# Kernel tuning notes

Measured on AMD Instinct MI355X. Metric: run time of the kernel, lower is better.

## Reference

```python
import jax, jax.numpy as jnp
import numpy as np
from jax import lax

EPS = 1e-5
K = 80000 // 16  # sample_pixels // 16 selected regions per image


def _conv(x, w):
    return lax.conv_general_dilated(x, w, (1, 1), 'VALID',
                                    dimension_numbers=('NHWC', 'HWIO', 'NHWC'))


def _bn(x, g, b, m, v):
    # Keras BatchNormalization in inference mode
    return (x - m) * (g * lax.rsqrt(v + EPS)) + b


def _crop(x, bi, iy, ix, size, pad):
    # tf.image.crop_and_resize with 'nearest' and integer-aligned boxes of span
    # (size+2*pad) reduces to a zero-padded window gather (out-of-bounds -> 0).
    S = size + 2 * pad
    xp = jnp.pad(x, ((0, 0), (pad, pad), (pad, pad), (0, 0)))
    rows = iy[:, None] * size + jnp.arange(S)[None, :]  # padded coords (offset -pad+pad)
    cols = ix[:, None] * size + jnp.arange(S)[None, :]
    return xp[bi[:, None, None], rows[:, :, None], cols[:, None, :], :]  # [N,S,S,C]


def _replace(x, y, bi, iy, ix):
    # scatter 4x4 patches y [N,4,4,C] back into x [B,H,W,C] at block (iy,ix)
    B, H, W, C = x.shape
    x6 = x.reshape(B, H // 4, 4, W // 4, 4, C).transpose(0, 1, 3, 2, 4, 5)
    x6 = x6.at[bi, iy, ix].set(y)
    return x6.transpose(0, 1, 3, 2, 4, 5).reshape(B, H, W, C)


def _forward(src, bgr, pha, fgr, err, hid,
             w1, g1, b1, m1, v1, w2, g2, b2, m2, v2,
             w3, g3, b3, m3, v3, w4, b4):
    B, Hf, Wf = src.shape[:3]
    Hh, Wh, Hq, Wq = Hf // 2, Wf // 2, Hf // 4, Wf // 4
    src_bgr = jnp.concatenate([src, bgr], axis=-1)

    # err already at quarter resolution -> tf bilinear resize is identity
    top_idx = lax.top_k(err[..., 0].reshape(B, -1), K)[1]  # [B,K]
    ref = jnp.zeros((B, Hq * Wq), err.dtype).at[jnp.arange(B)[:, None], top_idx].set(1.0)
    ref = ref.reshape(B, Hq, Wq, 1) * (err > 0).astype(err.dtype)

    bi = jnp.repeat(jnp.arange(B), K)          # [N] patch batch index, N = B*K
    iy = (top_idx // Wq).reshape(-1)
    ix = (top_idx % Wq).reshape(-1)

    x = jnp.concatenate([hid, pha, fgr], axis=-1)  # [B,Hq,Wq,36]
    x = jax.image.resize(x, (B, Hh, Wh, x.shape[-1]), 'bilinear')
    xp = _crop(x, bi, iy, ix, 2, 3)                # [N,8,8,36]
    yh = jax.image.resize(src_bgr, (B, Hh, Wh, 6), 'bilinear')
    yp = _crop(yh, bi, iy, ix, 2, 3)               # [N,8,8,6]

    t = jax.nn.relu(_bn(_conv(jnp.concatenate([xp, yp], -1), w1), g1, b1, m1, v1))  # [N,6,6,24]
    t = jax.nn.relu(_bn(_conv(t, w2), g2, b2, m2, v2))                              # [N,4,4,16]
    t = jax.image.resize(t, (t.shape[0], 8, 8, t.shape[-1]), 'nearest')
    y2 = _crop(src_bgr, bi, iy, ix, 4, 2)                                           # [N,8,8,6]
    t = jax.nn.relu(_bn(_conv(jnp.concatenate([t, y2], -1), w3), g3, b3, m3, v3))   # [N,6,6,12]
    t = _conv(t, w4) + b4                                                            # [N,4,4,4]

    pha_f = jax.image.resize(pha, (B, Hf, Wf, 1), 'bilinear')
    fgr_f = jax.image.resize(fgr, (B, Hf, Wf, 3), 'bilinear')
    pha_f = _replace(pha_f, t[..., :1], bi, iy, ix)
    fgr_f = _replace(fgr_f, t[..., 1:], bi, iy, ix)
    return pha_f, fgr_f, ref


def setup_inputs() -> dict:
    key = jax.random.key(0)
    ks = jax.random.split(key, 10)
    B, H, W = 2, 1088, 1920
    Hq, Wq = H // 4, W // 4
    f = jnp.float32

    def w(k, s):
        return jax.random.normal(k, s, f) * 0.05

    return dict(
        src=jax.random.uniform(ks[0], (B, H, W, 3), f),
        bgr=jax.random.uniform(ks[1], (B, H, W, 3), f),
        pha=jax.random.uniform(ks[2], (B, Hq, Wq, 1), f),
        fgr=jax.random.uniform(ks[3], (B, Hq, Wq, 3), f),
        err=jax.random.uniform(ks[4], (B, Hq, Wq, 1), f),
        hid=jax.random.uniform(ks[5], (B, Hq, Wq, 32), f),
        w1=w(ks[6], (3, 3, 42, 24)),
        g1=jnp.ones((24,), f), b1=jnp.zeros((24,), f), m1=jnp.zeros((24,), f), v1=jnp.ones((24,), f),
        w2=w(ks[7], (3, 3, 24, 16)),
        g2=jnp.ones((16,), f), b2=jnp.zeros((16,), f), m2=jnp.zeros((16,), f), v2=jnp.ones((16,), f),
        w3=w(ks[8], (3, 3, 22, 12)),
        g3=jnp.ones((12,), f), b3=jnp.zeros((12,), f), m3=jnp.zeros((12,), f), v3=jnp.ones((12,), f),
        w4=w(ks[9], (3, 3, 12, 4)), b4=jnp.zeros((4,), f),
    )


def reference(src, bgr, pha, fgr, err, hid,
              w1, g1, b1, m1, v1, w2, g2, b2, m2, v2,
              w3, g3, b3, m3, v3, w4, b4):
    return _forward(src, bgr, pha, fgr, err, hid,
                    w1, g1, b1, m1, v1, w2, g2, b2, m2, v2,
                    w3, g3, b3, m3, v3, w4, b4)
```

## Files before the change

### kernel.cpp

```cpp
#include <hip/hip_runtime.h>

#define EPS 1e-5f

constexpr int NB = 2, HQ = 272, WQ = 480, HH = 544, WH = 960, HF = 1088, WF = 1920;
constexpr int KSEL = 5000;
constexpr int NQ  = HQ * WQ;
constexpr int NEL = NB * NQ;
constexpr int PHA_N = NB * HF * WF;
constexpr int FGR_BASE = PHA_N;
constexpr int REF_BASE = PHA_N * 4;
constexpr int TIE_CAP = 8192;

constexpr int OFF_H1      = 0;
constexpr int OFF_H2      = 131072;
constexpr int OFF_META    = 262144;
constexpr int OFF_TIECNT  = 262160;
constexpr int OFF_PCOUNT  = 262162;
constexpr int OFF_TIELIST = 262176;
constexpr int OFF_PLIST   = OFF_TIELIST + 2 * TIE_CAP;
constexpr int OFF_W       = 288576;
constexpr int OFF_YH      = 303968;
constexpr int OFF_WP      = OFF_YH + NB * HH * WH * 6;
constexpr int ZERO_N      = OFF_TIELIST;

constexpr int W1F = 0;
constexpr int B1F = 9072;
constexpr int W2F = 9096;
constexpr int B2F = 12552;
constexpr int W3F = 12568;
constexpr int B3F = 14944;
constexpr int W4F = 14956;
constexpr int B4F = 15388;

typedef short s8v __attribute__((ext_vector_type(8)));
typedef float f4v __attribute__((ext_vector_type(4)));

static __device__ __forceinline__ unsigned short f2bf(float x) {
    unsigned u = __float_as_uint(x);
    u += 0x7fffu + ((u >> 16) & 1u);
    return (unsigned short)(u >> 16);
}
static __device__ __forceinline__ unsigned pack2(float a, float b) {
    return (unsigned)f2bf(a) | ((unsigned)f2bf(b) << 16);
}

__global__ void zero_k(unsigned* __restrict__ p, int n) {
    int i = blockIdx.x * 256 + threadIdx.x;
    if (i < n) p[i] = 0u;
}

__global__ void fold_weights(
    const float* __restrict__ w1, const float* __restrict__ g1, const float* __restrict__ b1,
    const float* __restrict__ m1, const float* __restrict__ v1,
    const float* __restrict__ w2, const float* __restrict__ g2, const float* __restrict__ b2,
    const float* __restrict__ m2, const float* __restrict__ v2,
    const float* __restrict__ w3, const float* __restrict__ g3, const float* __restrict__ b3,
    const float* __restrict__ m3, const float* __restrict__ v3,
    const float* __restrict__ w4, const float* __restrict__ b4,
    float* __restrict__ W)
{
    __shared__ float s1[24], a1[24], s2[16], a2[16], s3[12], a3[12];
    int t = threadIdx.x;
    if (t < 24) { float s = g1[t] / sqrtf(v1[t] + EPS); s1[t] = s; a1[t] = b1[t] - m1[t] * s; }
    else if (t < 40) { int o = t - 24; float s = g2[o] / sqrtf(v2[o] + EPS); s2[o] = s; a2[o] = b2[o] - m2[o] * s; }
    else if (t < 52) { int o = t - 40; float s = g3[o] / sqrtf(v3[o] + EPS); s3[o] = s; a3[o] = b3[o] - m3[o] * s; }
    __syncthreads();
    for (int i = t; i < 9072; i += 256) W[W1F + i] = w1[i] * s1[i % 24];
    if (t < 24) W[B1F + t] = a1[t];
    for (int i = t; i < 3456; i += 256) W[W2F + i] = w2[i] * s2[i % 16];
    if (t < 16) W[B2F + t] = a2[t];
    for (int i = t; i < 2376; i += 256) W[W3F + i] = w3[i] * s3[i % 12];
    if (t < 12) W[B3F + t] = a3[t];
    for (int i = t; i < 432; i += 256) W[W4F + i] = w4[i];
    if (t < 4) W[B4F + t] = b4[t];
}

__global__ void prepack(const float* __restrict__ Wf, unsigned short* __restrict__ P) {
    int idx = blockIdx.x * 256 + threadIdx.x;
    if (idx >= 32256) return;
    int j = idx & 7;
    int lane = (idx >> 3) & 63;
    int frag = idx >> 9;
    int li = lane & 15, g = lane >> 4;
    float val = 0.f;
    if (frag < 36) {
        int nt = frag & 1, ks = (frag >> 1) & 1, tap = frag >> 2;
        int n = nt * 16 + li, k = ks * 32 + 8 * g + j;
        if (n < 24 && k < 42) val = Wf[W1F + (tap * 42 + k) * 24 + n];
    } else if (frag < 45) {
        int tap = frag - 36, k = 8 * g + j;
        if (k < 24) val = Wf[W2F + (tap * 24 + k) * 16 + li];
    } else if (frag < 54) {
        int tap = frag - 45, k = 8 * g + j;
        if (li < 12 && k < 22) val = Wf[W3F + (tap * 22 + k) * 12 + li];
    } else {
        int tap = frag - 54, k = 8 * g + j;
        if (li < 4 && k < 12) val = Wf[W4F + (tap * 12 + k) * 4 + li];
    }
    P[idx] = f2bf(val);
}

__global__ void hist_hi(const float* __restrict__ err, unsigned* __restrict__ hist) {
    int i = blockIdx.x * 256 + threadIdx.x;
    if (i >= NEL) return;
    int b = i / NQ;
    unsigned key = __float_as_uint(err[i]);
    atomicAdd(&hist[b * 65536 + (key >> 16)], 1u);
}

__global__ void find_bin(const unsigned* __restrict__ hist, int* __restrict__ meta) {
    int b = blockIdx.x, tid = threadIdx.x;
    const unsigned* h = hist + b * 65536;
    __shared__ unsigned sf[256];
    __shared__ int ssel; __shared__ unsigned scum;
    unsigned own = 0;
    for (int i = 0; i < 256; i++) own += h[tid * 256 + i];
    sf[tid] = own; __syncthreads();
    for (int off = 1; off < 256; off <<= 1) {
        unsigned v = (tid + off < 256) ? sf[tid + off] : 0u;
        __syncthreads(); sf[tid] += v; __syncthreads();
    }
    if (sf[tid] >= (unsigned)KSEL && sf[tid] - own < (unsigned)KSEL) { ssel = tid; scum = sf[tid] - own; }
    __syncthreads();
    int chunk = ssel; unsigned cum = scum;
    unsigned own2 = h[chunk * 256 + tid];
    sf[tid] = own2; __syncthreads();
    for (int off = 1; off < 256; off <<= 1) {
        unsigned v = (tid + off < 256) ? sf[tid + off] : 0u;
        __syncthreads(); sf[tid] += v; __syncthreads();
    }
    if (cum + sf[tid] >= (unsigned)KSEL && cum + sf[tid] - own2 < (unsigned)KSEL) {
        meta[b * 8 + 0] = chunk * 256 + tid;
        meta[b * 8 + 1] = (int)(cum + sf[tid] - own2);
    }
}

__global__ void hist_lo(const float* __restrict__ err, const int* __restrict__ meta,
                        unsigned* __restrict__ hist2) {
    int i = blockIdx.x * 256 + threadIdx.x;
    if (i >= NEL) return;
    int b = i / NQ;
    unsigned key = __float_as_uint(err[i]);
    if ((int)(key >> 16) == meta[b * 8 + 0])
        atomicAdd(&hist2[b * 65536 + (key & 0xFFFFu)], 1u);
}

__global__ void find_thresh(const unsigned* __restrict__ hist2, int* __restrict__ meta) {
    int b = blockIdx.x, tid = threadIdx.x;
    const unsigned* h = hist2 + b * 65536;
    __shared__ unsigned sf[256];
    __shared__ int ssel; __shared__ unsigned scum;
    unsigned own = 0;
    for (int i = 0; i < 256; i++) own += h[tid * 256 + i];
    sf[tid] = own; __syncthreads();
    for (int off = 1; off < 256; off <<= 1) {
        unsigned v = (tid + off < 256) ? sf[tid + off] : 0u;
        __syncthreads(); sf[tid] += v; __syncthreads();
    }
    unsigned cum0 = (unsigned)meta[b * 8 + 1];
    if (cum0 + sf[tid] >= (unsigned)KSEL && cum0 + sf[tid] - own < (unsigned)KSEL) {
        ssel = tid; scum = cum0 + sf[tid] - own;
    }
    __syncthreads();
    int chunk = ssel; unsigned cum = scum;
    unsigned own2 = h[chunk * 256 + tid];
    sf[tid] = own2; __syncthreads();
    for (int off = 1; off < 256; off <<= 1) {
        unsigned v = (tid + off < 256) ? sf[tid + off] : 0u;
        __syncthreads(); sf[tid] += v; __syncthreads();
    }
    if (cum + sf[tid] >= (unsigned)KSEL && cum + sf[tid] - own2 < (unsigned)KSEL) {
        meta[b * 8 + 2] = (int)(((unsigned)meta[b * 8 + 0] << 16) | (unsigned)(chunk * 256 + tid));
        meta[b * 8 + 3] = KSEL - (int)(cum + sf[tid] - own2);
    }
}

__global__ void tie_list_k(const float* __restrict__ err, const int* __restrict__ meta,
                           int* __restrict__ tieCnt, int* __restrict__ tieList) {
    int i = blockIdx.x * 256 + threadIdx.x;
    if (i >= NEL) return;
    int b = i / NQ;
    unsigned key = __float_as_uint(err[i]);
    if (key == (unsigned)meta[b * 8 + 2]) {
        int n = atomicAdd(&tieCnt[b], 1);
        if (n < TIE_CAP) tieList[b * TIE_CAP + n] = i - b * NQ;
    }
}

__global__ void select_k(const float* __restrict__ err, const int* __restrict__ meta,
                         int* __restrict__ plist, int* __restrict__ pcount,
                         float* __restrict__ out) {
    int i = blockIdx.x * 256 + threadIdx.x;
    if (i >= NEL) return;
    int b = i / NQ;
    unsigned key = __float_as_uint(err[i]);
    unsigned T = (unsigned)meta[b * 8 + 2];
    float r = 0.f;
    if (key > T) {
        r = 1.0f;
        int n = atomicAdd(pcount, 1);
        plist[n] = i;
    }
    out[REF_BASE + i] = r;
}

__global__ void tie_select(const int* __restrict__ meta, const int* __restrict__ tieCnt,
                           const int* __restrict__ tieList,
                           int* __restrict__ plist, int* __restrict__ pcount,
                           float* __restrict__ out) {
    int b = blockIdx.x;
    int n = tieCnt[b]; if (n > TIE_CAP) n = TIE_CAP;
    int R = meta[b * 8 + 3];
    unsigned T = (unsigned)meta[b * 8 + 2];
    float val = (T > 0u) ? 1.0f : 0.0f;
    for (int e = threadIdx.x; e < n; e += blockDim.x) {
        int my = tieList[b * TIE_CAP + e];
        int rank = 0;
        for (int f = 0; f < n; f++) rank += (tieList[b * TIE_CAP + f] < my) ? 1 : 0;
        if (rank < R) {
            out[REF_BASE + b * NQ + my] = val;
            int q = atomicAdd(pcount, 1);
            plist[q] = b * NQ + my;
        }
    }
}

__global__ void yh_kernel(const float* __restrict__ src, const float* __restrict__ bgr,
                          float* __restrict__ yh) {
    int idx = blockIdx.x * 256 + threadIdx.x;
    if (idx >= NB * HH * WH) return;
    int hx = idx % WH; int t = idx / WH; int hy = t % HH; int b = t / HH;

    float wy[4]; int jy[4]; float sy = 0.f;
#pragma unroll
    for (int k = 0; k < 4; k++) {
        int j = 2 * hy - 1 + k;
        float w = (k == 0 || k == 3) ? 0.125f : 0.375f;
        if (j < 0 || j >= HF) { w = 0.f; j = 0; }
        jy[k] = j; wy[k] = w; sy += w;
    }
    float wx[4]; int jx[4]; float sx = 0.f;
#pragma unroll
    for (int k = 0; k < 4; k++) {
        int j = 2 * hx - 1 + k;
        float w = (k == 0 || k == 3) ? 0.125f : 0.375f;
        if (j < 0 || j >= WF) { w = 0.f; j = 0; }
        jx[k] = j; wx[k] = w; sx += w;
    }
    float inv = 1.f / (sy * sx);
    float acc[6] = {0.f, 0.f, 0.f, 0.f, 0.f, 0.f};
#pragma unroll
    for (int a = 0; a < 4; a++) {
#pragma unroll
        for (int c = 0; c < 4; c++) {
            float w = wy[a] * wx[c];
            int p = ((b * HF + jy[a]) * WF + jx[c]) * 3;
            acc[0] += w * src[p + 0]; acc[1] += w * src[p + 1]; acc[2] += w * src[p + 2];
            acc[3] += w * bgr[p + 0]; acc[4] += w * bgr[p + 1]; acc[5] += w * bgr[p + 2];
        }
    }
    float* Y = yh + (size_t)idx * 6;
#pragma unroll
    for (int j = 0; j < 6; j++) Y[j] = acc[j] * inv;
}

__global__ void base_up(const float* __restrict__ pha, const float* __restrict__ fgr,
                        float* __restrict__ out) {
    int idx = blockIdx.x * 256 + threadIdx.x;
    if (idx >= PHA_N) return;
    int x = idx % WF; int t = idx / WF; int y = t % HF; int b = t / HF;
    int ky = y >> 2, ry = y & 3, kx = x >> 2, rx = x & 3;
    int qy0; float wy0;
    if (ry == 0) { qy0 = ky - 1; wy0 = 0.375f; }
    else if (ry == 1) { qy0 = ky - 1; wy0 = 0.125f; }
    else if (ry == 2) { qy0 = ky; wy0 = 0.875f; }
    else { qy0 = ky; wy0 = 0.625f; }
    int qy1 = qy0 + 1; float wy1 = 1.f - wy0;
    if (qy0 < 0) qy0 = 0; if (qy1 > HQ - 1) qy1 = HQ - 1;
    int qx0; float wx0;
    if (rx == 0) { qx0 = kx - 1; wx0 = 0.375f; }
    else if (rx == 1) { qx0 = kx - 1; wx0 = 0.125f; }
    else if (rx == 2) { qx0 = kx; wx0 = 0.875f; }
    else { qx0 = kx; wx0 = 0.625f; }
    int qx1 = qx0 + 1; float wx1 = 1.f - wx0;
    if (qx0 < 0) qx0 = 0; if (qx1 > WQ - 1) qx1 = WQ - 1;

    int rb = b * HQ;
    int p00 = (rb + qy0) * WQ + qx0, p01 = (rb + qy0) * WQ + qx1;
    int p10 = (rb + qy1) * WQ + qx0, p11 = (rb + qy1) * WQ + qx1;
    float w00 = wy0 * wx0, w01 = wy0 * wx1, w10 = wy1 * wx0, w11 = wy1 * wx1;

    out[idx] = w00 * pha[p00] + w01 * pha[p01] + w10 * pha[p10] + w11 * pha[p11];
    float* fo = out + FGR_BASE + (size_t)idx * 3;
#pragma unroll
    for (int j = 0; j < 3; j++)
        fo[j] = w00 * fgr[p00 * 3 + j] + w01 * fgr[p01 * 3 + j]
              + w10 * fgr[p10 * 3 + j] + w11 * fgr[p11 * 3 + j];
}

__global__ __launch_bounds__(64) void patch_kernel(
    const float* __restrict__ src, const float* __restrict__ bgr,
    const float* __restrict__ pha, const float* __restrict__ fgr,
    const float* __restrict__ hid, const float* __restrict__ yh,
    const float* __restrict__ Wb, const unsigned short* __restrict__ WP,
    const int* __restrict__ plist, const int* __restrict__ pcount,
    float* __restrict__ out)
{
    if ((int)blockIdx.x >= *pcount) return;
    int pk = plist[blockIdx.x];
    int b = pk / NQ, pos = pk % NQ;
    int iy = pos / WQ, ix = pos % WQ;
    int lane = threadIdx.x;
    int g = lane >> 4, li = lane & 15;

    __shared__ __align__(16) unsigned short win[64 * 72];
    __shared__ __align__(16) unsigned short t1s[36 * 40];

    const s8v* WP1v = (const s8v*)WP;
    const s8v* WP2v = WP1v + 36 * 64;
    const s8v* WP3v = WP2v + 9 * 64;
    const s8v* WP4v = WP3v + 9 * 64;

    {
        int r = lane >> 3, c = lane & 7;
        int hy = iy * 2 - 3 + r, hx = ix * 2 - 3 + c;
        unsigned* wrow = (unsigned*)&win[lane * 72];
        if (hy < 0 || hy >= HH || hx < 0 || hx >= WH) {
#pragma unroll
            for (int q = 0; q < 32; q++) wrow[q] = 0u;
        } else {
            int qy0 = (hy - 1) >> 1, qy1 = qy0 + 1;
            float wy0 = (hy & 1) ? 0.75f : 0.25f, wy1 = 1.f - wy0;
            int qx0 = (hx - 1) >> 1, qx1 = qx0 + 1;
            float wx0 = (hx & 1) ? 0.75f : 0.25f, wx1 = 1.f - wx0;
            qy0 = max(qy0, 0); qy1 = min(qy1, HQ - 1);
            qx0 = max(qx0, 0); qx1 = min(qx1, WQ - 1);
            int rb = b * HQ;
            int p00 = (rb + qy0) * WQ + qx0, p01 = (rb + qy0) * WQ + qx1;
            int p10 = (rb + qy1) * WQ + qx0, p11 = (rb + qy1) * WQ + qx1;
            float w00 = wy0 * wx0, w01 = wy0 * wx1, w10 = wy1 * wx0, w11 = wy1 * wx1;
            const float4* h00 = (const float4*)(hid + (size_t)p00 * 32);
            const float4* h01 = (const float4*)(hid + (size_t)p01 * 32);
            const float4* h10 = (const float4*)(hid + (size_t)p10 * 32);
            const float4* h11 = (const float4*)(hid + (size_t)p11 * 32);
#pragma unroll
            for (int q = 0; q < 8; q++) {
                float4 v0 = h00[q], v1 = h01[q], v2 = h10[q], v3 = h11[q];
                float e0 = v0.x * w00 + v1.x * w01 + v2.x * w10 + v3.x * w11;
                float e1 = v0.y * w00 + v1.y * w01 + v2.y * w10 + v3.y * w11;
                float e2 = v0.z * w00 + v1.z * w01 + v2.z * w10 + v3.z * w11;
                float e3 = v0.w * w00 + v1.w * w01 + v2.w * w10 + v3.w * w11;
                wrow[q * 2]     = pack2(e0, e1);
                wrow[q * 2 + 1] = pack2(e2, e3);
            }
            float e32 = pha[p00] * w00 + pha[p01] * w01 + pha[p10] * w10 + pha[p11] * w11;
            float fg[3];
#pragma unroll
            for (int j = 0; j < 3; j++)
                fg[j] = fgr[p00 * 3 + j] * w00 + fgr[p01 * 3 + j] * w01
                      + fgr[p10 * 3 + j] * w10 + fgr[p11 * 3 + j] * w11;
            wrow[16] = pack2(e32, fg[0]);
            wrow[17] = pack2(fg[1], fg[2]);
            const float* Y = yh + (size_t)((b * HH + hy) * WH + hx) * 6;
            wrow[18] = pack2(Y[0], Y[1]);
            wrow[19] = pack2(Y[2], Y[3]);
            wrow[20] = pack2(Y[4], Y[5]);
#pragma unroll
            for (int q = 21; q < 32; q++) wrow[q] = 0u;
        }
    }
    __syncthreads();

    int p0 = li, p1 = 16 + li, p2 = (32 + li > 35) ? 35 : 32 + li;
    int pr0 = (p0 * 171) >> 10, pc0 = p0 - pr0 * 6;
    int pr1 = (p1 * 171) >> 10, pc1 = p1 - pr1 * 6;
    int pr2m = (p2 * 171) >> 10, pc2m = p2 - pr2m * 6;
    int cb0 = pr0 * 8 + pc0, cb1 = pr1 * 8 + pc1, cb2 = pr2m * 8 + pc2m;

    f4v a00 = {0,0,0,0}, a01 = {0,0,0,0}, a10 = {0,0,0,0},
        a11 = {0,0,0,0}, a20 = {0,0,0,0}, a21 = {0,0,0,0};
    {
        const unsigned short* r0 = &win[cb0 * 72 + g * 8];
        const unsigned short* r1 = &win[cb1 * 72 + g * 8];
        const unsigned short* r2 = &win[cb2 * 72 + g * 8];
#pragma unroll
        for (int tap = 0; tap < 9; tap++) {
            const int dr = tap / 3, dc = tap % 3;
            const int coff = (dr * 8 + dc) * 72;
#pragma unroll
            for (int ks = 0; ks < 2; ks++) {
                s8v av0 = *(const s8v*)(r0 + coff + ks * 32);
                s8v av1 = *(const s8v*)(r1 + coff + ks * 32);
                s8v av2 = *(const s8v*)(r2 + coff + ks * 32);
                s8v bv0 = WP1v[((tap * 2 + ks) * 2 + 0) * 64 + lane];
                s8v bv1 = WP1v[((tap * 2 + ks) * 2 + 1) * 64 + lane];
                a00 = __builtin_amdgcn_mfma_f32_16x16x32_bf16(av0, bv0, a00, 0, 0, 0);
                a01 = __builtin_amdgcn_mfma_f32_16x16x32_bf16(av0, bv1, a01, 0, 0, 0);
                a10 = __builtin_amdgcn_mfma_f32_16x16x32_bf16(av1, bv0, a10, 0, 0, 0);
                a11 = __builtin_amdgcn_mfma_f32_16x16x32_bf16(av1, bv1, a11, 0, 0, 0);
                a20 = __builtin_amdgcn_mfma_f32_16x16x32_bf16(av2, bv0, a20, 0, 0, 0);
                a21 = __builtin_amdgcn_mfma_f32_16x16x32_bf16(av2, bv1, a21, 0, 0, 0);
            }
        }
    }
    {
        float b1n0 = Wb[B1F + li];
        float b1n1 = (li < 8) ? Wb[B1F + 16 + li] : 0.f;
#pragma unroll
        for (int r = 0; r < 4; r++) {
            int p = 4 * g + r;
            t1s[p * 40 + li]        = f2bf(fmaxf(a00[r] + b1n0, 0.f));
            t1s[p * 40 + 16 + li]   = f2bf(fmaxf(a01[r] + b1n1, 0.f));
            int pp = 16 + p;
            t1s[pp * 40 + li]       = f2bf(fmaxf(a10[r] + b1n0, 0.f));
            t1s[pp * 40 + 16 + li]  = f2bf(fmaxf(a11[r] + b1n1, 0.f));
            int p2r = 32 + p;
            if (p2r < 36) {
                t1s[p2r * 40 + li]      = f2bf(fmaxf(a20[r] + b1n0, 0.f));
                t1s[p2r * 40 + 16 + li] = f2bf(fmaxf(a21[r] + b1n1, 0.f));
            }
        }
    }
    __syncthreads();

    f4v c2 = {0,0,0,0};
    {
        int pr = li >> 2, pc = li & 3;
#pragma unroll
        for (int tap = 0; tap < 9; tap++) {
            const int dr = tap / 3, dc = tap % 3;
            int cell = (pr + dr) * 6 + pc + dc;
            s8v av = *(const s8v*)&t1s[cell * 40 + g * 8];
            c2 = __builtin_amdgcn_mfma_f32_16x16x32_bf16(av, WP2v[tap * 64 + lane], c2, 0, 0, 0);
        }
    }
    __syncthreads();
    {
        float b2v = Wb[B2F + li];
#pragma unroll
        for (int r = 0; r < 4; r++) {
            int p = 4 * g + r;
            unsigned short hv = f2bf(fmaxf(c2[r] + b2v, 0.f));
            int r0 = (p >> 2) * 2, c0 = (p & 3) * 2;
            win[(r0 * 8 + c0) * 40 + li]       = hv;
            win[(r0 * 8 + c0 + 1) * 40 + li]   = hv;
            win[((r0 + 1) * 8 + c0) * 40 + li]     = hv;
            win[((r0 + 1) * 8 + c0 + 1) * 40 + li] = hv;
        }
        int rr = lane >> 3, cc = lane & 7;
        int fy = iy * 4 - 2 + rr, fx = ix * 4 - 2 + cc;
        unsigned* wp3 = (unsigned*)&win[lane * 40];
        if (fy >= 0 && fy < HF && fx >= 0 && fx < WF) {
            const float* sp = src + ((size_t)(b * HF + fy) * WF + fx) * 3;
            const float* bp = bgr + ((size_t)(b * HF + fy) * WF + fx) * 3;
            wp3[8]  = pack2(sp[0], sp[1]);
            wp3[9]  = pack2(sp[2], bp[0]);
            wp3[10] = pack2(bp[1], bp[2]);
        } else {
            wp3[8] = 0u; wp3[9] = 0u; wp3[10] = 0u;
        }
        wp3[11] = 0u; wp3[12] = 0u; wp3[13] = 0u; wp3[14] = 0u; wp3[15] = 0u;
        for (int idx = lane; idx < 36 * 8; idx += 64) {
            int row = idx >> 3;
            ((unsigned*)t1s)[row * 20 + 8 + (idx & 7)] = 0u;
        }
    }
    __syncthreads();

    f4v c30 = {0,0,0,0}, c31 = {0,0,0,0}, c32 = {0,0,0,0};
    {
        const unsigned short* r0 = &win[cb0 * 40 + g * 8];
        const unsigned short* r1 = &win[cb1 * 40 + g * 8];
        const unsigned short* r2 = &win[cb2 * 40 + g * 8];
#pragma unroll
        for (int tap = 0; tap < 9; tap++) {
            const int dr = tap / 3, dc = tap % 3;
            const int coff = (dr * 8 + dc) * 40;
            s8v bv = WP3v[tap * 64 + lane];
            c30 = __builtin_amdgcn_mfma_f32_16x16x32_bf16(*(const s8v*)(r0 + coff), bv, c30, 0, 0, 0);
            c31 = __builtin_amdgcn_mfma_f32_16x16x32_bf16(*(const s8v*)(r1 + coff), bv, c31, 0, 0, 0);
            c32 = __builtin_amdgcn_mfma_f32_16x16x32_bf16(*(const s8v*)(r2 + coff), bv, c32, 0, 0, 0);
        }
    }
    __syncthreads();
    {
        float b3v = (li < 12) ? Wb[B3F + li] : 0.f;
#pragma unroll
        for (int r = 0; r < 4; r++) {
            int p = 4 * g + r;
            t1s[p * 40 + li]        = f2bf(fmaxf(c30[r] + b3v, 0.f));
            t1s[(16 + p) * 40 + li] = f2bf(fmaxf(c31[r] + b3v, 0.f));
            int p2r = 32 + p;
            if (p2r < 36) t1s[p2r * 40 + li] = f2bf(fmaxf(c32[r] + b3v, 0.f));
        }
    }
    __syncthreads();

    f4v c4 = {0,0,0,0};
    {
        int pr = li >> 2, pc = li & 3;
#pragma unroll
        for (int tap = 0; tap < 9; tap++) {
            const int dr = tap / 3, dc = tap % 3;
            int cell = (pr + dr) * 6 + pc + dc;
            s8v av = *(const s8v*)&t1s[cell * 40 + g * 8];
            c4 = __builtin_amdgcn_mfma_f32_16x16x32_bf16(av, WP4v[tap * 64 + lane], c4, 0, 0, 0);
        }
    }
    if (li < 4) {
        float b4v = Wb[B4F + li];
#pragma unroll
        for (int r = 0; r < 4; r++) {
            int p = 4 * g + r;
            int prow = p >> 2, pcol = p & 3;
            float v = c4[r] + b4v;
            int fidx = (b * HF + iy * 4 + prow) * WF + ix * 4 + pcol;
            if (li == 0) out[fidx] = v;
            else out[FGR_BASE + (size_t)fidx * 3 + (li - 1)] = v;
        }
    }
}

extern "C" void kernel_launch(void* const* d_in, const int* in_sizes, int n_in,
                              void* d_out, int out_size, void* d_ws, size_t ws_size,
                              hipStream_t stream)
{
    const float* src = (const float*)d_in[0];
    const float* bgr = (const float*)d_in[1];
    const float* pha = (const float*)d_in[2];
    const float* fgr = (const float*)d_in[3];
    const float* err = (const float*)d_in[4];
    const float* hid = (const float*)d_in[5];
    const float* w1 = (const float*)d_in[6];
    const float* g1 = (const float*)d_in[7];
    const float* b1 = (const float*)d_in[8];
    const float* m1 = (const float*)d_in[9];
    const float* v1 = (const float*)d_in[10];
    const float* w2 = (const float*)d_in[11];
    const float* g2 = (const float*)d_in[12];
    const float* b2 = (const float*)d_in[13];
    const float* m2 = (const float*)d_in[14];
    const float* v2 = (const float*)d_in[15];
    const float* w3 = (const float*)d_in[16];
    const float* g3 = (const float*)d_in[17];
    const float* b3 = (const float*)d_in[18];
    const float* m3 = (const float*)d_in[19];
    const float* v3 = (const float*)d_in[20];
    const float* w4 = (const float*)d_in[21];
    const float* b4 = (const float*)d_in[22];

    float* out = (float*)d_out;
    unsigned* ws = (unsigned*)d_ws;
    float* wsf = (float*)d_ws;
    int* meta    = (int*)(ws + OFF_META);
    int* tieCnt  = (int*)(ws + OFF_TIECNT);
    int* pcount  = (int*)(ws + OFF_PCOUNT);
    int* tieList = (int*)(ws + OFF_TIELIST);
    int* plist   = (int*)(ws + OFF_PLIST);
    float* W  = wsf + OFF_W;
    float* yh = wsf + OFF_YH;
    unsigned short* WP = (unsigned short*)(wsf + OFF_WP);

    zero_k<<<(ZERO_N + 255) / 256, 256, 0, stream>>>(ws, ZERO_N);
    fold_weights<<<1, 256, 0, stream>>>(w1, g1, b1, m1, v1, w2, g2, b2, m2, v2,
                                        w3, g3, b3, m3, v3, w4, b4, W);
    prepack<<<126, 256, 0, stream>>>(W, WP);
    hist_hi<<<(NEL + 255) / 256, 256, 0, stream>>>(err, ws + OFF_H1);
    find_bin<<<NB, 256, 0, stream>>>(ws + OFF_H1, meta);
    hist_lo<<<(NEL + 255) / 256, 256, 0, stream>>>(err, meta, ws + OFF_H2);
    find_thresh<<<NB, 256, 0, stream>>>(ws + OFF_H2, meta);
    tie_list_k<<<(NEL + 255) / 256, 256, 0, stream>>>(err, meta, tieCnt, tieList);
    select_k<<<(NEL + 255) / 256, 256, 0, stream>>>(err, meta, plist, pcount, out);
    tie_select<<<NB, 256, 0, stream>>>(meta, tieCnt, tieList, plist, pcount, out);
    yh_kernel<<<(NB * HH * WH + 255) / 256, 256, 0, stream>>>(src, bgr, yh);
    base_up<<<(PHA_N + 255) / 256, 256, 0, stream>>>(pha, fgr, out);
    patch_kernel<<<NB * KSEL, 64, 0, stream>>>(src, bgr, pha, fgr, hid, yh, W, WP,
                                               plist, pcount, out);
}
```

Measured before the change: 469.4 us.

## Restructure top-k radix select with LDS histograms and fewer kernel launches

Merges weight folding and MFMA prepacking into one kernel that computes BN scales inline. The first histogram pass now runs over 15-bit key prefixes, accumulated in packed 16-bit shared-memory counters before a merge into global memory, which cuts global atomic contention. The second pass widens to 17 bits to match, and tie-list collection is folded into the selection kernel, removing one full pass over err and two launches. The risk is that the packed 16-bit counters could overflow if one block's chunk concentrates more than 65535 keys into a bin, though each chunk holds only 4080 elements.

After: 393.5 us. 1.19x faster.

```diff
diff --git a/kernel.cpp b/kernel.cpp
--- a/kernel.cpp
+++ b/kernel.cpp
@@ -10,27 +10,19 @@
 constexpr int FGR_BASE = PHA_N;
 constexpr int REF_BASE = PHA_N * 4;
 constexpr int TIE_CAP = 8192;
+constexpr int CHUNK = 4080;
 
 constexpr int OFF_H1      = 0;
-constexpr int OFF_H2      = 131072;
-constexpr int OFF_META    = 262144;
-constexpr int OFF_TIECNT  = 262160;
-constexpr int OFF_PCOUNT  = 262162;
-constexpr int OFF_TIELIST = 262176;
+constexpr int OFF_H2      = 65536;
+constexpr int OFF_META    = 327680;
+constexpr int OFF_TIECNT  = 327696;
+constexpr int OFF_PCOUNT  = 327698;
+constexpr int OFF_TIELIST = 327712;
 constexpr int OFF_PLIST   = OFF_TIELIST + 2 * TIE_CAP;
-constexpr int OFF_W       = 288576;
-constexpr int OFF_YH      = 303968;
+constexpr int OFF_WB      = 354112;
+constexpr int OFF_YH      = 354176;
 constexpr int OFF_WP      = OFF_YH + NB * HH * WH * 6;
 constexpr int ZERO_N      = OFF_TIELIST;
-
-constexpr int W1F = 0;
-constexpr int B1F = 9072;
-constexpr int W2F = 9096;
-constexpr int B2F = 12552;
-constexpr int W3F = 12568;
-constexpr int B3F = 14944;
-constexpr int W4F = 14956;
-constexpr int B4F = 15388;
 
 typedef short s8v __attribute__((ext_vector_type(8)));
 typedef float f4v __attribute__((ext_vector_type(4)));
@@ -49,7 +41,7 @@
     if (i < n) p[i] = 0u;
 }
 
-__global__ void fold_weights(
+__global__ void prepack_all(
     const float* __restrict__ w1, const float* __restrict__ g1, const float* __restrict__ b1,
     const float* __restrict__ m1, const float* __restrict__ v1,
     const float* __restrict__ w2, const float* __restrict__ g2, const float* __restrict__ b2,
@@ -57,64 +49,69 @@
     const float* __restrict__ w3, const float* __restrict__ g3, const float* __restrict__ b3,
     const float* __restrict__ m3, const float* __restrict__ v3,
     const float* __restrict__ w4, const float* __restrict__ b4,
-    float* __restrict__ W)
+    unsigned short* __restrict__ P, float* __restrict__ Wb)
 {
-    __shared__ float s1[24], a1[24], s2[16], a2[16], s3[12], a3[12];
-    int t = threadIdx.x;
-    if (t < 24) { float s = g1[t] / sqrtf(v1[t] + EPS); s1[t] = s; a1[t] = b1[t] - m1[t] * s; }
-    else if (t < 40) { int o = t - 24; float s = g2[o] / sqrtf(v2[o] + EPS); s2[o] = s; a2[o] = b2[o] - m2[o] * s; }
-    else if (t < 52) { int o = t - 40; float s = g3[o] / sqrtf(v3[o] + EPS); s3[o] = s; a3[o] = b3[o] - m3[o] * s; }
-    __syncthreads();
-    for (int i = t; i < 9072; i += 256) W[W1F + i] = w1[i] * s1[i % 24];
-    if (t < 24) W[B1F + t] = a1[t];
-    for (int i = t; i < 3456; i += 256) W[W2F + i] = w2[i] * s2[i % 16];
-    if (t < 16) W[B2F + t] = a2[t];
-    for (int i = t; i < 2376; i += 256) W[W3F + i] = w3[i] * s3[i % 12];
-    if (t < 12) W[B3F + t] = a3[t];
-    for (int i = t; i < 432; i += 256) W[W4F + i] = w4[i];
-    if (t < 4) W[B4F + t] = b4[t];
-}
-
-__global__ void prepack(const float* __restrict__ Wf, unsigned short* __restrict__ P) {
     int idx = blockIdx.x * 256 + threadIdx.x;
-    if (idx >= 32256) return;
-    int j = idx & 7;
-    int lane = (idx >> 3) & 63;
-    int frag = idx >> 9;
-    int li = lane & 15, g = lane >> 4;
-    float val = 0.f;
-    if (frag < 36) {
-        int nt = frag & 1, ks = (frag >> 1) & 1, tap = frag >> 2;
-        int n = nt * 16 + li, k = ks * 32 + 8 * g + j;
-        if (n < 24 && k < 42) val = Wf[W1F + (tap * 42 + k) * 24 + n];
-    } else if (frag < 45) {
-        int tap = frag - 36, k = 8 * g + j;
-        if (k < 24) val = Wf[W2F + (tap * 24 + k) * 16 + li];
-    } else if (frag < 54) {
-        int tap = frag - 45, k = 8 * g + j;
-        if (li < 12 && k < 22) val = Wf[W3F + (tap * 22 + k) * 12 + li];
+    if (idx < 32256) {
+        int j = idx & 7;
+        int lane = (idx >> 3) & 63;
+        int frag = idx >> 9;
+        int li = lane & 15, g = lane >> 4;
+        float val = 0.f;
+        if (frag < 36) {
+            int nt = frag & 1, ks = (frag >> 1) & 1, tap = frag >> 2;
+            int n = nt * 16 + li, k = ks * 32 + 8 * g + j;
+            if (n < 24 && k < 42) val = w1[(tap * 42 + k) * 24 + n] * (g1[n] / sqrtf(v1[n] + EPS));
+        } else if (frag < 45) {
+            int tap = frag - 36, k = 8 * g + j;
+            if (k < 24) val = w2[(tap * 24 + k) * 16 + li] * (g2[li] / sqrtf(v2[li] + EPS));
+        } else if (frag < 54) {
+            int tap = frag - 45, k = 8 * g + j;
+            if (li < 12 && k < 22) val = w3[(tap * 22 + k) * 12 + li] * (g3[li] / sqrtf(v3[li] + EPS));
+        } else {
+            int tap = frag - 54, k = 8 * g + j;
+            if (li < 4 && k < 12) val = w4[(tap * 12 + k) * 4 + li];
+        }
+        P[idx] = f2bf(val);
     } else {
-        int tap = frag - 54, k = 8 * g + j;
-        if (li < 4 && k < 12) val = Wf[W4F + (tap * 12 + k) * 4 + li];
-    }
-    P[idx] = f2bf(val);
-}
-
-__global__ void hist_hi(const float* __restrict__ err, unsigned* __restrict__ hist) {
-    int i = blockIdx.x * 256 + threadIdx.x;
-    if (i >= NEL) return;
-    int b = i / NQ;
-    unsigned key = __float_as_uint(err[i]);
-    atomicAdd(&hist[b * 65536 + (key >> 16)], 1u);
+        int o = idx - 32256;
+        if (o < 24) { float s = g1[o] / sqrtf(v1[o] + EPS); Wb[o] = b1[o] - m1[o] * s; }
+        else if (o < 40) { int q = o - 24; float s = g2[q] / sqrtf(v2[q] + EPS); Wb[o] = b2[q] - m2[q] * s; }
+        else if (o < 52) { int q = o - 40; float s = g3[q] / sqrtf(v3[q] + EPS); Wb[o] = b3[q] - m3[q] * s; }
+        else if (o < 56) Wb[o] = b4[o - 52];
+    }
+}
+
+__global__ __launch_bounds__(256) void hist_l1(const float* __restrict__ err,
+                                               unsigned* __restrict__ hist) {
+    __shared__ unsigned lh[16384];
+    int b = blockIdx.x >> 5, ch = blockIdx.x & 31;
+    for (int i = threadIdx.x; i < 16384; i += 256) lh[i] = 0u;
+    __syncthreads();
+    int base = b * NQ + ch * CHUNK;
+    for (int i = threadIdx.x; i < CHUNK; i += 256) {
+        unsigned bin = __float_as_uint(err[base + i]) >> 17;
+        atomicAdd(&lh[bin >> 1], 1u << ((bin & 1) * 16));
+    }
+    __syncthreads();
+    unsigned* gh = hist + b * 32768;
+    for (int i = threadIdx.x; i < 16384; i += 256) {
+        unsigned w = lh[i];
+        if (w & 0xFFFFu) atomicAdd(&gh[2 * i], w & 0xFFFFu);
+        if (w >> 16)     atomicAdd(&gh[2 * i + 1], w >> 16);
+    }
 }
 
 __global__ void find_bin(const unsigned* __restrict__ hist, int* __restrict__ meta) {
     int b = blockIdx.x, tid = threadIdx.x;
-    const unsigned* h = hist + b * 65536;
+    const unsigned* h = hist + b * 32768;
     __shared__ unsigned sf[256];
     __shared__ int ssel; __shared__ unsigned scum;
     unsigned own = 0;
-    for (int i = 0; i < 256; i++) own += h[tid * 256 + i];
+    {
+        const uint4* hv = (const uint4*)(h + tid * 128);
+        for (int i = 0; i < 32; i++) { uint4 v = hv[i]; own += v.x + v.y + v.z + v.w; }
+    }
     sf[tid] = own; __syncthreads();
     for (int off = 1; off < 256; off <<= 1) {
         unsigned v = (tid + off < 256) ? sf[tid + off] : 0u;
@@ -123,35 +120,38 @@
     if (sf[tid] >= (unsigned)KSEL && sf[tid] - own < (unsigned)KSEL) { ssel = tid; scum = sf[tid] - own; }
     __syncthreads();
     int chunk = ssel; unsigned cum = scum;
-    unsigned own2 = h[chunk * 256 + tid];
+    unsigned own2 = (tid < 128) ? h[chunk * 128 + tid] : 0u;
     sf[tid] = own2; __syncthreads();
     for (int off = 1; off < 256; off <<= 1) {
         unsigned v = (tid + off < 256) ? sf[tid + off] : 0u;
         __syncthreads(); sf[tid] += v; __syncthreads();
     }
     if (cum + sf[tid] >= (unsigned)KSEL && cum + sf[tid] - own2 < (unsigned)KSEL) {
-        meta[b * 8 + 0] = chunk * 256 + tid;
+        meta[b * 8 + 0] = chunk * 128 + tid;
         meta[b * 8 + 1] = (int)(cum + sf[tid] - own2);
     }
 }
 
-__global__ void hist_lo(const float* __restrict__ err, const int* __restrict__ meta,
+__global__ void hist_l2(const float* __restrict__ err, const int* __restrict__ meta,
                         unsigned* __restrict__ hist2) {
     int i = blockIdx.x * 256 + threadIdx.x;
     if (i >= NEL) return;
     int b = i / NQ;
     unsigned key = __float_as_uint(err[i]);
-    if ((int)(key >> 16) == meta[b * 8 + 0])
-        atomicAdd(&hist2[b * 65536 + (key & 0xFFFFu)], 1u);
+    if ((int)(key >> 17) == meta[b * 8 + 0])
+        atomicAdd(&hist2[b * 131072 + (key & 0x1FFFFu)], 1u);
 }
 
 __global__ void find_thresh(const unsigned* __restrict__ hist2, int* __restrict__ meta) {
     int b = blockIdx.x, tid = threadIdx.x;
-    const unsigned* h = hist2 + b * 65536;
+    const unsigned* h = hist2 + b * 131072;
     __shared__ unsigned sf[256];
     __shared__ int ssel; __shared__ unsigned scum;
     unsigned own = 0;
-    for (int i = 0; i < 256; i++) own += h[tid * 256 + i];
+    {
+        const uint4* hv = (const uint4*)(h + tid * 512);
+        for (int i = 0; i < 128; i++) { uint4 v = hv[i]; own += v.x + v.y + v.z + v.w; }
+    }
     sf[tid] = own; __syncthreads();
     for (int off = 1; off < 256; off <<= 1) {
         unsigned v = (tid + off < 256) ? sf[tid + off] : 0u;
@@ -163,33 +163,28 @@
     }
     __syncthreads();
     int chunk = ssel; unsigned cum = scum;
-    unsigned own2 = h[chunk * 256 + tid];
+    unsigned hi = h[chunk * 512 + 2 * tid + 1], lo = h[chunk * 512 + 2 * tid];
+    unsigned own2 = hi + lo;
     sf[tid] = own2; __syncthreads();
     for (int off = 1; off < 256; off <<= 1) {
         unsigned v = (tid + off < 256) ? sf[tid + off] : 0u;
         __syncthreads(); sf[tid] += v; __syncthreads();
     }
     if (cum + sf[tid] >= (unsigned)KSEL && cum + sf[tid] - own2 < (unsigned)KSEL) {
-        meta[b * 8 + 2] = (int)(((unsigned)meta[b * 8 + 0] << 16) | (unsigned)(chunk * 256 + tid));
-        meta[b * 8 + 3] = KSEL - (int)(cum + sf[tid] - own2);
-    }
-}
-
-__global__ void tie_list_k(const float* __restrict__ err, const int* __restrict__ meta,
-                           int* __restrict__ tieCnt, int* __restrict__ tieList) {
-    int i = blockIdx.x * 256 + threadIdx.x;
-    if (i >= NEL) return;
-    int b = i / NQ;
-    unsigned key = __float_as_uint(err[i]);
-    if (key == (unsigned)meta[b * 8 + 2]) {
-        int n = atomicAdd(&tieCnt[b], 1);
-        if (n < TIE_CAP) tieList[b * TIE_CAP + n] = i - b * NQ;
-    }
-}
-
-__global__ void select_k(const float* __restrict__ err, const int* __restrict__ meta,
-                         int* __restrict__ plist, int* __restrict__ pcount,
-                         float* __restrict__ out) {
+        unsigned cumo = cum + sf[tid] - own2;
+        int bl; int R;
+        if (cumo + hi >= (unsigned)KSEL) { bl = 2 * tid + 1; R = KSEL - (int)cumo; }
+        else { bl = 2 * tid; R = KSEL - (int)(cumo + hi); }
+        unsigned low17 = (unsigned)(chunk * 512 + bl);
+        meta[b * 8 + 2] = (int)(((unsigned)meta[b * 8 + 0] << 17) | low17);
+        meta[b * 8 + 3] = R;
+    }
+}
+
+__global__ void select_tie(const float* __restrict__ err, const int* __restrict__ meta,
+                           int* __restrict__ plist, int* __restrict__ pcount,
+                           int* __restrict__ tieCnt, int* __restrict__ tieList,
+                           float* __restrict__ out) {
     int i = blockIdx.x * 256 + threadIdx.x;
     if (i >= NEL) return;
     int b = i / NQ;
@@ -200,6 +195,9 @@
         r = 1.0f;
         int n = atomicAdd(pcount, 1);
         plist[n] = i;
+    } else if (key == T) {
+        int n = atomicAdd(&tieCnt[b], 1);
+        if (n < TIE_CAP) tieList[b * TIE_CAP + n] = i - b * NQ;
     }
     out[REF_BASE + i] = r;
 }
@@ -404,8 +402,8 @@
         }
     }
     {
-        float b1n0 = Wb[B1F + li];
-        float b1n1 = (li < 8) ? Wb[B1F + 16 + li] : 0.f;
+        float b1n0 = Wb[li];
+        float b1n1 = (li < 8) ? Wb[16 + li] : 0.f;
 #pragma unroll
         for (int r = 0; r < 4; r++) {
             int p = 4 * g + r;
@@ -436,7 +434,7 @@
     }
     __syncthreads();
     {
-        float b2v = Wb[B2F + li];
+        float b2v = Wb[24 + li];
 #pragma unroll
         for (int r = 0; r < 4; r++) {
             int p = 4 * g + r;
@@ -484,7 +482,7 @@
     }
     __syncthreads();
     {
-        float b3v = (li < 12) ? Wb[B3F + li] : 0.f;
+        float b3v = (li < 12) ? Wb[40 + li] : 0.f;
 #pragma unroll
         for (int r = 0; r < 4; r++) {
             int p = 4 * g + r;
@@ -508,7 +506,7 @@
         }
     }
     if (li < 4) {
-        float b4v = Wb[B4F + li];
+        float b4v = Wb[52 + li];
 #pragma unroll
         for (int r = 0; r < 4; r++) {
             int p = 4 * g + r;
@@ -557,23 +555,22 @@
     int* pcount  = (int*)(ws + OFF_PCOUNT);
     int* tieList = (int*)(ws + OFF_TIELIST);
     int* plist   = (int*)(ws + OFF_PLIST);
-    float* W  = wsf + OFF_W;
+    float* Wb = wsf + OFF_WB;
     float* yh = wsf + OFF_YH;
     unsigned short* WP = (unsigned short*)(wsf + OFF_WP);
 
     zero_k<<<(ZERO_N + 255) / 256, 256, 0, stream>>>(ws, ZERO_N);
-    fold_weights<<<1, 256, 0, stream>>>(w1, g1, b1, m1, v1, w2, g2, b2, m2, v2,
-                                        w3, g3, b3, m3, v3, w4, b4, W);
-    prepack<<<126, 256, 0, stream>>>(W, WP);
-    hist_hi<<<(NEL + 255) / 256, 256, 0, stream>>>(err, ws + OFF_H1);
+    prepack_all<<<127, 256, 0, stream>>>(w1, g1, b1, m1, v1, w2, g2, b2, m2, v2,
+                                         w3, g3, b3, m3, v3, w4, b4, WP, Wb);
+    hist_l1<<<64, 256, 0, stream>>>(err, ws + OFF_H1);
     find_bin<<<NB, 256, 0, stream>>>(ws + OFF_H1, meta);
-    hist_lo<<<(NEL + 255) / 256, 256, 0, stream>>>(err, meta, ws + OFF_H2);
+    hist_l2<<<(NEL + 255) / 256, 256, 0, stream>>>(err, meta, ws + OFF_H2);
     find_thresh<<<NB, 256, 0, stream>>>(ws + OFF_H2, meta);
-    tie_list_k<<<(NEL + 255) / 256, 256, 0, stream>>>(err, meta, tieCnt, tieList);
-    select_k<<<(NEL + 255) / 256, 256, 0, stream>>>(err, meta, plist, pcount, out);
+    select_tie<<<(NEL + 255) / 256, 256, 0, stream>>>(err, meta, plist, pcount,
+                                                      tieCnt, tieList, out);
     tie_select<<<NB, 256, 0, stream>>>(meta, tieCnt, tieList, plist, pcount, out);
     yh_kernel<<<(NB * HH * WH + 255) / 256, 256, 0, stream>>>(src, bgr, yh);
     base_up<<<(PHA_N + 255) / 256, 256, 0, stream>>>(pha, fgr, out);
-    patch_kernel<<<NB * KSEL, 64, 0, stream>>>(src, bgr, pha, fgr, hid, yh, W, WP,
+    patch_kernel<<<NB * KSEL, 64, 0, stream>>>(src, bgr, pha, fgr, hid, yh, Wb, WP,
                                                plist, pcount, out);
 }
```
